# Optimization experiments

Hardware: AMD Instinct MI355X
Metric: run time of the kernel (lower is better)

The kernel has to match this reference:

```python
import jax, jax.numpy as jnp
import numpy as np

B, L, D, H, Dh = 4, 2048, 1024, 16, 64
DECAY_LR, A_LR, V_LR, G_LR = 64, 64, 32, 128
EPS_GN = 0.00064


def _lora(x, A, Bm, b, act):
    h = x @ A.T
    if act is not None:
        h = act(h)
    y = h @ Bm.T
    return y if b is None else y + b


def setup_inputs() -> dict:
    key = jax.random.key(0)
    ks = jax.random.split(key, 32)
    n = lambda k, shape, s=0.02: (jax.random.normal(k, shape, jnp.float32) * s)
    return {
        "x": n(ks[0], (B, L, D), 1.0),
        "v_first": n(ks[1], (B, L, H, Dh), 1.0),
        "x_r": n(ks[2], (1, 1, D)), "x_w": n(ks[3], (1, 1, D)),
        "x_k": n(ks[4], (1, 1, D)), "x_v": n(ks[5], (1, 1, D)),
        "x_a": n(ks[6], (1, 1, D)), "x_g": n(ks[7], (1, 1, D)),
        "k_k": n(ks[8], (H, Dh), 0.5), "k_a": n(ks[9], (H, Dh), 0.5),
        "r_k": n(ks[10], (H, Dh), 0.5),
        "Wr": n(ks[11], (D, D)), "Wk": n(ks[12], (D, D)),
        "Wv": n(ks[13], (D, D)), "Wo": n(ks[14], (D, D)),
        "gn_w": 1.0 + n(ks[15], (H, Dh)), "gn_b": n(ks[16], (H, Dh)),
        "w_A": n(ks[17], (DECAY_LR, D)), "w_B": n(ks[18], (D, DECAY_LR)), "w_b": n(ks[19], (D,)),
        "v_A": n(ks[20], (V_LR, D)), "v_B": n(ks[21], (D, V_LR)), "v_b": n(ks[22], (D,)),
        "a_A": n(ks[23], (A_LR, D)), "a_B": n(ks[24], (D, A_LR)), "a_b": n(ks[25], (D,)),
        "g_A": n(ks[26], (G_LR, D)), "g_B": n(ks[27], (D, G_LR)),
    }


def reference(x, v_first, x_r, x_w, x_k, x_v, x_a, x_g, k_k, k_a, r_k,
              Wr, Wk, Wv, Wo, gn_w, gn_b,
              w_A, w_B, w_b, v_A, v_B, v_b, a_A, a_B, a_b, g_A, g_B):
    Bx, Lx, Dx = x.shape
    # token shift (no cache -> zero-padded shift)
    x_prev = jnp.concatenate([jnp.zeros_like(x[:, :1]), x[:, :-1]], axis=1)
    xx = x_prev - x
    xr = x + xx * x_r
    xw = x + xx * x_w
    xk = x + xx * x_k
    xv = x + xx * x_v
    xa = x + xx * x_a
    xg = x + xx * x_g

    r = (xr @ Wr.T).reshape(Bx, Lx, H, Dh)
    k = (xk @ Wk.T).reshape(Bx, Lx, H, Dh)
    v = (xv @ Wv.T).reshape(Bx, Lx, H, Dh)
    iclr = jax.nn.sigmoid(_lora(xa, a_A, a_B, a_b, None)).reshape(Bx, Lx, H, Dh)
    gate = _lora(xg, g_A, g_B, None, jax.nn.sigmoid)  # (B,L,D)

    # layer_idx > 0: residual value mixing with v_first
    vv = jax.nn.sigmoid(_lora(xv, v_A, v_B, v_b, None)).reshape(Bx, Lx, H, Dh)
    v = v + (v_first - v) * vv

    w = jnp.exp(-0.606531 * jax.nn.sigmoid(
        _lora(xw, w_A, w_B, w_b, jnp.tanh)).reshape(Bx, Lx, H, Dh))

    kkn = k * k_k
    kk = kkn / jnp.maximum(jnp.linalg.norm(kkn, axis=-1, keepdims=True), 1e-7)
    k = k * (1.0 + (iclr - 1.0) * k_a)
    a = -kk
    b = kk * iclr

    # WKV7 generalized delta-rule scan over time
    def step(state, inp):
        rt, wt, kt, vt, at, bt = inp  # each (B,H,Dh)
        sa = jnp.einsum('bhij,bhj->bhi', state, at)
        state = (state * wt[:, :, None, :]
                 + vt[..., :, None] * kt[..., None, :]
                 + sa[..., :, None] * bt[..., None, :])
        y = jnp.einsum('bhij,bhj->bhi', state, rt)
        return state, y

    tr = lambda z: jnp.swapaxes(z, 0, 1)  # (B,L,H,Dh) -> (L,B,H,Dh)
    state0 = jnp.zeros((Bx, H, Dh, Dh), x.dtype)
    _, ys = jax.lax.scan(step, state0, (tr(r), tr(w), tr(k), tr(v), tr(a), tr(b)))
    out = jnp.swapaxes(ys, 0, 1)  # (B,L,H,Dh)

    # per-head layernorm (group norm), eps = 0.00064
    mean = out.mean(axis=-1, keepdims=True)
    var = out.var(axis=-1, keepdims=True)
    out = gn_w * (out - mean) / jnp.sqrt(var + EPS_GN) + gn_b

    out = out + jnp.sum(r * k * r_k, axis=-1, keepdims=True) * v
    out = out.reshape(Bx, Lx, Dx)
    return (out * gate) @ Wo.T
```

## Files before the change

### kernel.cpp

```cpp
#include <hip/hip_runtime.h>
#include <cmath>


#define DEV __device__ __forceinline__

typedef unsigned short u16;
typedef unsigned int u32;
typedef __bf16 bf16x8 __attribute__((ext_vector_type(8)));
typedef float f32x4 __attribute__((ext_vector_type(4)));

constexpr int Bx = 4, Lx = 2048, Dx = 1024, Hx = 16, Dh = 64;
constexpr int NTOK = Bx * Lx;
constexpr float EPS_GN = 0.00064f;
constexpr int STEP_U16 = 384;
constexpr int TB = 16;
constexpr int NB = Lx / TB;
constexpr int BATCH_U16 = TB * STEP_U16;

DEV float bf2f(u16 u) { union { u32 i; float f; } c; c.i = ((u32)u) << 16; return c.f; }
DEV u16 f2bf(float f) {
    union { float f; u32 i; } c; c.f = f;
    u32 r = c.i + 0x7FFFu + ((c.i >> 16) & 1u);
    return (u16)(r >> 16);
}
DEV void unpack2(u32 u, float& a, float& b) {
    union { u32 i; float f; } c0, c1;
    c0.i = u << 16; c1.i = u & 0xFFFF0000u;
    a = c0.f; b = c1.f;
}

template <int CTRL>
DEV float dpp_add(float v) {
    int p = __builtin_amdgcn_update_dpp(0, __float_as_int(v), CTRL, 0xF, 0xF, true);
    return v + __int_as_float(p);
}

DEV float xor32_add(float x) {
    float a = x, b = x;
    asm volatile("s_nop 1\n\tv_permlane32_swap_b32 %0, %1" : "+v"(a), "+v"(b));
    return a + b;
}

DEV float red32(float x) {
    x = dpp_add<0xB1>(x);
    x = dpp_add<0x4E>(x);
    x = dpp_add<0x141>(x);
    x = dpp_add<0x140>(x);
    return xor32_add(x);
}

__global__ __launch_bounds__(256) void convmix_kernel(
    const float* __restrict__ x,
    const float* __restrict__ mr, const float* __restrict__ mw, const float* __restrict__ mk,
    const float* __restrict__ mv, const float* __restrict__ ma, const float* __restrict__ mg,
    u16* __restrict__ XR, u16* __restrict__ XW, u16* __restrict__ XK,
    u16* __restrict__ XV, u16* __restrict__ XA, u16* __restrict__ XG,
    const float* s0, const float* s1, const float* s2, const float* s3,
    const float* s4, const float* s5, const float* s6, const float* s7,
    const float* s8, const float* s9, const float* s10, const float* s11,
    u16* d0, u16* d1, u16* d2, u16* d3, u16* d4, u16* d5, u16* d6, u16* d7,
    u16* d8, u16* d9, u16* d10, u16* d11)
{
    const int bid = blockIdx.x;
    const int tid = threadIdx.x;
    if (bid < 8192) {
        int gi = bid * 256 + tid;
        int n  = gi >> 8;
        int d4v = (gi & 255) << 2;
        int l  = n & (Lx - 1);
        size_t o = (size_t)n * Dx + d4v;
        float4 xc = *(const float4*)(x + o);
        float4 xp = make_float4(0.f, 0.f, 0.f, 0.f);
        if (l != 0) xp = *(const float4*)(x + o - Dx);
        float dx0 = xp.x - xc.x, dx1 = xp.y - xc.y, dx2 = xp.z - xc.z, dx3 = xp.w - xc.w;
        const float* mvs[6] = {mr, mw, mk, mv, ma, mg};
        u16* dsts[6] = {XR, XW, XK, XV, XA, XG};
#pragma unroll
        for (int j = 0; j < 6; ++j) {
            float4 m = *(const float4*)(mvs[j] + d4v);
            ushort4 r;
            r.x = f2bf(fmaf(dx0, m.x, xc.x));
            r.y = f2bf(fmaf(dx1, m.y, xc.y));
            r.z = f2bf(fmaf(dx2, m.z, xc.z));
            r.w = f2bf(fmaf(dx3, m.w, xc.w));
            *(ushort4*)(dsts[j] + o) = r;
        }
    } else {
        const float* srcs[12] = {s0,s1,s2,s3,s4,s5,s6,s7,s8,s9,s10,s11};
        u16* dsts[12] = {d0,d1,d2,d3,d4,d5,d6,d7,d8,d9,d10,d11};
        const int ns[12] = {65536,65536,32768,32768,65536,65536,131072,131072,
                            1048576,1048576,1048576,1048576};
        int cb = bid - 8192;
        int t = cb >> 10;
        int i = ((cb & 1023) * 256 + tid) * 4;
        if (i >= ns[t]) return;
        float4 v = *(const float4*)(srcs[t] + i);
        ushort4 o;
        o.x = f2bf(v.x); o.y = f2bf(v.y); o.z = f2bf(v.z); o.w = f2bf(v.w);
        *(ushort4*)(dsts[t] + i) = o;
    }
}

template <int BN, int ACT, bool BIAS, bool F32OUT>
DEV void gemm_body(u16* __restrict__ smem,
                   const u16* __restrict__ A, const u16* __restrict__ B16,
                   const float* __restrict__ bias, void* __restrict__ Cv,
                   int M, int N, int K, int bx, int by)
{
    constexpr int BM = 128, BK = 32;
    constexpr int WGM = (BN == 128) ? 2 : 4;
    constexpr int WGN = (BN == 128) ? 2 : 1;
    constexpr int WTM = BM / WGM, WTN = BN / WGN;
    constexpr int ITM = WTM / 16, ITN = WTN / 16;
    u16* Asm0 = smem;
    u16* Bsm0 = smem + 2 * BM * BK;
    const int tid = threadIdx.x;
    const int wid = tid >> 6, lane = tid & 63;
    const int q = lane >> 4, r16 = lane & 15;
    const size_t m0 = (size_t)bx * BM;
    const size_t n0 = (size_t)by * BN;
    const int wm = (wid % WGM) * WTM;
    const int wn = (wid / WGM) * WTN;
    f32x4 acc[ITM][ITN];
    const f32x4 zf = {0.f, 0.f, 0.f, 0.f};
#pragma unroll
    for (int i = 0; i < ITM; ++i)
#pragma unroll
        for (int j = 0; j < ITN; ++j) acc[i][j] = zf;

#pragma unroll
    for (int it = 0; it < 2; ++it) {
        int base = it * 2048 + wid * 512;
        int pp = base + lane * 8;
        int row = pp >> 5, col = pp & 31;
        __builtin_amdgcn_global_load_lds(
            (const __attribute__((address_space(1))) void*)(A + (m0 + row) * K + col),
            (__attribute__((address_space(3))) void*)(Asm0 + base), 16, 0, 0);
    }
#pragma unroll
    for (int it = 0; it < (BN * BK + 2047) / 2048; ++it) {
        int base = it * 2048 + wid * 512;
        if (BN * BK >= 2048 || base < BN * BK) {
            int pp = base + lane * 8;
            int row = pp >> 5, col = pp & 31;
            __builtin_amdgcn_global_load_lds(
                (const __attribute__((address_space(1))) void*)(B16 + (n0 + row) * K + col),
                (__attribute__((address_space(3))) void*)(Bsm0 + base), 16, 0, 0);
        }
    }

    int t = 0;
    for (int k0 = 0; k0 < K; k0 += BK, ++t) {
        const int cur = t & 1;
        __syncthreads();
        if (k0 + BK < K) {
            u16* An = Asm0 + (cur ^ 1) * (BM * BK);
            u16* Bn = Bsm0 + (cur ^ 1) * (BN * BK);
            const int kn = k0 + BK;
#pragma unroll
            for (int it = 0; it < 2; ++it) {
                int base = it * 2048 + wid * 512;
                int pp = base + lane * 8;
                int row = pp >> 5, col = pp & 31;
                __builtin_amdgcn_global_load_lds(
                    (const __attribute__((address_space(1))) void*)(A + (m0 + row) * K + kn + col),
                    (__attribute__((address_space(3))) void*)(An + base), 16, 0, 0);
            }
#pragma unroll
            for (int it = 0; it < (BN * BK + 2047) / 2048; ++it) {
                int base = it * 2048 + wid * 512;
                if (BN * BK >= 2048 || base < BN * BK) {
                    int pp = base + lane * 8;
                    int row = pp >> 5, col = pp & 31;
                    __builtin_amdgcn_global_load_lds(
                        (const __attribute__((address_space(1))) void*)(B16 + (n0 + row) * K + kn + col),
                        (__attribute__((address_space(3))) void*)(Bn + base), 16, 0, 0);
                }
            }
        }
        const u16* Ac = Asm0 + cur * (BM * BK);
        const u16* Bc = Bsm0 + cur * (BN * BK);
        bf16x8 af[ITM], bfr[ITN];
#pragma unroll
        for (int im = 0; im < ITM; ++im)
            af[im] = *(const bf16x8*)&Ac[(wm + im * 16 + r16) * BK + q * 8];
#pragma unroll
        for (int in = 0; in < ITN; ++in)
            bfr[in] = *(const bf16x8*)&Bc[(wn + in * 16 + r16) * BK + q * 8];
#pragma unroll
        for (int im = 0; im < ITM; ++im)
#pragma unroll
            for (int in = 0; in < ITN; ++in)
                acc[im][in] = __builtin_amdgcn_mfma_f32_16x16x32_bf16(af[im], bfr[in], acc[im][in], 0, 0, 0);
    }
#pragma unroll
    for (int im = 0; im < ITM; ++im) {
#pragma unroll
        for (int in = 0; in < ITN; ++in) {
#pragma unroll
            for (int e = 0; e < 4; ++e) {
                size_t row = m0 + wm + im * 16 + q * 4 + e;
                size_t col = n0 + wn + in * 16 + r16;
                float val = acc[im][in][e];
                if constexpr (BIAS) val += bias[col];
                if constexpr (ACT == 1) val = 1.f / (1.f + __expf(-val));
                else if constexpr (ACT == 2) val = tanhf(val);
                else if constexpr (ACT == 3) val = __expf(-0.606531f / (1.f + __expf(-val)));
                if constexpr (F32OUT) ((float*)Cv)[row * (size_t)N + col] = val;
                else ((u16*)Cv)[row * (size_t)N + col] = f2bf(val);
            }
        }
    }
}

DEV void gemm_body_rt(u16* __restrict__ smem,
                      const u16* __restrict__ A, const u16* __restrict__ B16,
                      const float* __restrict__ bias, u16* __restrict__ C,
                      int N, int K, int act, int bx, int by)
{
    constexpr int BM = 128, BK = 32;
    constexpr int ITM = 4, ITN = 4;
    u16* Asm0 = smem;
    u16* Bsm0 = smem + 2 * BM * BK;
    const int tid = threadIdx.x;
    const int wid = tid >> 6, lane = tid & 63;
    const int q = lane >> 4, r16 = lane & 15;
    const size_t m0 = (size_t)bx * BM;
    const size_t n0 = (size_t)by * 128;
    const int wm = (wid % 2) * 64;
    const int wn = (wid / 2) * 64;
    f32x4 acc[ITM][ITN];
    const f32x4 zf = {0.f, 0.f, 0.f, 0.f};
#pragma unroll
    for (int i = 0; i < ITM; ++i)
#pragma unroll
        for (int j = 0; j < ITN; ++j) acc[i][j] = zf;

#pragma unroll
    for (int it = 0; it < 2; ++it) {
        int base = it * 2048 + wid * 512;
        int pp = base + lane * 8;
        int row = pp >> 5, col = pp & 31;
        __builtin_amdgcn_global_load_lds(
            (const __attribute__((address_space(1))) void*)(A + (m0 + row) * K + col),
            (__attribute__((address_space(3))) void*)(Asm0 + base), 16, 0, 0);
        __builtin_amdgcn_global_load_lds(
            (const __attribute__((address_space(1))) void*)(B16 + (n0 + row) * K + col),
            (__attribute__((address_space(3))) void*)(Bsm0 + base), 16, 0, 0);
    }

    int t = 0;
    for (int k0 = 0; k0 < K; k0 += BK, ++t) {
        const int cur = t & 1;
        __syncthreads();
        if (k0 + BK < K) {
            u16* An = Asm0 + (cur ^ 1) * (BM * BK);
            u16* Bn = Bsm0 + (cur ^ 1) * (BM * BK);
            const int kn = k0 + BK;
#pragma unroll
            for (int it = 0; it < 2; ++it) {
                int base = it * 2048 + wid * 512;
                int pp = base + lane * 8;
                int row = pp >> 5, col = pp & 31;
                __builtin_amdgcn_global_load_lds(
                    (const __attribute__((address_space(1))) void*)(A + (m0 + row) * K + kn + col),
                    (__attribute__((address_space(3))) void*)(An + base), 16, 0, 0);
                __builtin_amdgcn_global_load_lds(
                    (const __attribute__((address_space(1))) void*)(B16 + (n0 + row) * K + kn + col),
                    (__attribute__((address_space(3))) void*)(Bn + base), 16, 0, 0);
            }
        }
        const u16* Ac = Asm0 + cur * (BM * BK);
        const u16* Bc = Bsm0 + cur * (BM * BK);
        bf16x8 af[ITM], bfr[ITN];
#pragma unroll
        for (int im = 0; im < ITM; ++im)
            af[im] = *(const bf16x8*)&Ac[(wm + im * 16 + r16) * BK + q * 8];
#pragma unroll
        for (int in = 0; in < ITN; ++in)
            bfr[in] = *(const bf16x8*)&Bc[(wn + in * 16 + r16) * BK + q * 8];
#pragma unroll
        for (int im = 0; im < ITM; ++im)
#pragma unroll
            for (int in = 0; in < ITN; ++in)
                acc[im][in] = __builtin_amdgcn_mfma_f32_16x16x32_bf16(af[im], bfr[in], acc[im][in], 0, 0, 0);
    }
#pragma unroll
    for (int im = 0; im < ITM; ++im) {
#pragma unroll
        for (int in = 0; in < ITN; ++in) {
#pragma unroll
            for (int e = 0; e < 4; ++e) {
                size_t row = m0 + wm + im * 16 + q * 4 + e;
                size_t col = n0 + wn + in * 16 + r16;
                float val = acc[im][in][e];
                if (bias) val += bias[col];
                if (act == 1) val = 1.f / (1.f + __expf(-val));
                else if (act == 3) val = __expf(-0.606531f / (1.f + __expf(-val)));
                C[row * (size_t)N + col] = f2bf(val);
            }
        }
    }
}

DEV void lora1_body(u16* __restrict__ smem, int cfg,
    const u16* __restrict__ XW, const u16* __restrict__ XA,
    const u16* __restrict__ XV, const u16* __restrict__ XG,
    const u16* __restrict__ wAB, const u16* __restrict__ aAB,
    const u16* __restrict__ vAB, const u16* __restrict__ gAB,
    u16* __restrict__ HW, u16* __restrict__ HA,
    u16* __restrict__ HV, u16* __restrict__ HG, int bx)
{
    constexpr int BM = 128, BK = 32, K = 1024;
    constexpr int ITM = 2, ITN = 4;
    const u16* A; const u16* Bm; u16* C; int ldC, Nv, act;
    if (cfg == 0)      { A = XW; Bm = wAB;            C = HW;      ldC = 64;  Nv = 64; act = 2; }
    else if (cfg == 1) { A = XA; Bm = aAB;            C = HA;      ldC = 64;  Nv = 64; act = 0; }
    else if (cfg == 2) { A = XV; Bm = vAB;            C = HV;      ldC = 32;  Nv = 32; act = 0; }
    else if (cfg == 3) { A = XG; Bm = gAB;            C = HG;      ldC = 128; Nv = 64; act = 1; }
    else               { A = XG; Bm = gAB + 64 * K;   C = HG + 64; ldC = 128; Nv = 64; act = 1; }

    u16* Asm0 = smem;
    u16* Bsm0 = smem + 2 * BM * BK;
    const int tid = threadIdx.x;
    const int wid = tid >> 6, lane = tid & 63;
    const int q = lane >> 4, r16 = lane & 15;
    const size_t m0 = (size_t)bx * BM;
    const int wm = wid * 32;
    f32x4 acc[ITM][ITN];
    const f32x4 zf = {0.f, 0.f, 0.f, 0.f};
#pragma unroll
    for (int i = 0; i < ITM; ++i)
#pragma unroll
        for (int j = 0; j < ITN; ++j) acc[i][j] = zf;

#pragma unroll
    for (int it = 0; it < 2; ++it) {
        int base = it * 2048 + wid * 512;
        int pp = base + lane * 8;
        int row = pp >> 5, col = pp & 31;
        __builtin_amdgcn_global_load_lds(
            (const __attribute__((address_space(1))) void*)(A + (m0 + row) * K + col),
            (__attribute__((address_space(3))) void*)(Asm0 + base), 16, 0, 0);
    }
    {
        int base = wid * 512;
        int pp = base + lane * 8;
        int row = pp >> 5, col = pp & 31;
        __builtin_amdgcn_global_load_lds(
            (const __attribute__((address_space(1))) void*)(Bm + row * K + col),
            (__attribute__((address_space(3))) void*)(Bsm0 + base), 16, 0, 0);
    }

    int t = 0;
    for (int k0 = 0; k0 < K; k0 += BK, ++t) {
        const int cur = t & 1;
        __syncthreads();
        if (k0 + BK < K) {
            u16* An = Asm0 + (cur ^ 1) * (BM * BK);
            u16* Bn = Bsm0 + (cur ^ 1) * 2048;
            const int kn = k0 + BK;
#pragma unroll
            for (int it = 0; it < 2; ++it) {
                int base = it * 2048 + wid * 512;
                int pp = base + lane * 8;
                int row = pp >> 5, col = pp & 31;
                __builtin_amdgcn_global_load_lds(
                    (const __attribute__((address_space(1))) void*)(A + (m0 + row) * K + kn + col),
                    (__attribute__((address_space(3))) void*)(An + base), 16, 0, 0);
            }
            {
                int base = wid * 512;
                int pp = base + lane * 8;
                int row = pp >> 5, col = pp & 31;
                __builtin_amdgcn_global_load_lds(
                    (const __attribute__((address_space(1))) void*)(Bm + row * K + kn + col),
                    (__attribute__((address_space(3))) void*)(Bn + base), 16, 0, 0);
            }
        }
        const u16* Ac = Asm0 + cur * (BM * BK);
        const u16* Bc = Bsm0 + cur * 2048;
        bf16x8 af[ITM], bfr[ITN];
#pragma unroll
        for (int im = 0; im < ITM; ++im)
            af[im] = *(const bf16x8*)&Ac[(wm + im * 16 + r16) * BK + q * 8];
#pragma unroll
        for (int in = 0; in < ITN; ++in)
            bfr[in] = *(const bf16x8*)&Bc[(in * 16 + r16) * BK + q * 8];
#pragma unroll
        for (int im = 0; im < ITM; ++im)
#pragma unroll
            for (int in = 0; in < ITN; ++in)
                acc[im][in] = __builtin_amdgcn_mfma_f32_16x16x32_bf16(af[im], bfr[in], acc[im][in], 0, 0, 0);
    }
#pragma unroll
    for (int im = 0; im < ITM; ++im) {
#pragma unroll
        for (int in = 0; in < ITN; ++in) {
#pragma unroll
            for (int e = 0; e < 4; ++e) {
                size_t row = m0 + wm + im * 16 + q * 4 + e;
                int col = in * 16 + r16;
                if (col < Nv) {
                    float val = acc[im][in][e];
                    if (act == 1) val = 1.f / (1.f + __expf(-val));
                    else if (act == 2) val = tanhf(val);
                    C[row * (size_t)ldC + col] = f2bf(val);
                }
            }
        }
    }
}

__global__ __launch_bounds__(256) void proj_kernel(
    const u16* __restrict__ XR, const u16* __restrict__ XK, const u16* __restrict__ XV,
    const u16* __restrict__ XW, const u16* __restrict__ XA, const u16* __restrict__ XG,
    const u16* __restrict__ Wr16, const u16* __restrict__ Wk16, const u16* __restrict__ Wv16,
    const u16* __restrict__ wAB, const u16* __restrict__ aAB,
    const u16* __restrict__ vAB, const u16* __restrict__ gAB,
    u16* __restrict__ Rbuf, u16* __restrict__ Kbuf, u16* __restrict__ Vbuf,
    u16* __restrict__ HW, u16* __restrict__ HA, u16* __restrict__ HV, u16* __restrict__ HG)
{
    __shared__ __align__(16) u16 pool[16384];
    const int z = blockIdx.z;
    if (z < 3) {
        const u16* A; const u16* Bm; u16* C;
        if (z == 0)      { A = XR; Bm = Wr16; C = Rbuf; }
        else if (z == 1) { A = XK; Bm = Wk16; C = Kbuf; }
        else             { A = XV; Bm = Wv16; C = Vbuf; }
        gemm_body<128, 0, false, false>(pool, A, Bm, nullptr, C, NTOK, 1024, 1024,
                                        blockIdx.x, blockIdx.y);
    } else {
        if (blockIdx.y >= 5) return;
        lora1_body(pool, blockIdx.y, XW, XA, XV, XG, wAB, aAB, vAB, gAB, HW, HA, HV, HG,
                   blockIdx.x);
    }
}

__global__ __launch_bounds__(256) void lora2_kernel(
    const u16* __restrict__ HW, const u16* __restrict__ HA,
    const u16* __restrict__ HV, const u16* __restrict__ HG,
    const u16* __restrict__ wBB, const u16* __restrict__ aBB,
    const u16* __restrict__ vBB, const u16* __restrict__ gBB,
    const float* __restrict__ wb, const float* __restrict__ ab, const float* __restrict__ vb,
    u16* __restrict__ Wdec16, u16* __restrict__ ICLR,
    u16* __restrict__ VVb, u16* __restrict__ GATE)
{
    __shared__ __align__(16) u16 pool[16384];
    const int z = blockIdx.z;
    const u16* A; const u16* Bm; const float* bias; u16* C; int K, act;
    if (z == 0)      { A = HW; Bm = wBB; bias = wb;      C = Wdec16; K = 64;  act = 3; }
    else if (z == 1) { A = HA; Bm = aBB; bias = ab;      C = ICLR;   K = 64;  act = 1; }
    else if (z == 2) { A = HV; Bm = vBB; bias = vb;      C = VVb;    K = 32;  act = 1; }
    else             { A = HG; Bm = gBB; bias = nullptr; C = GATE;   K = 128; act = 0; }
    gemm_body_rt(pool, A, Bm, bias, C, 1024, K, act, blockIdx.x, blockIdx.y);
}

__global__ __launch_bounds__(256) void gemm_out_kernel(
    const u16* __restrict__ A, const u16* __restrict__ B16, float* __restrict__ C)
{
    __shared__ __align__(16) u16 pool[16384];
    gemm_body<128, 0, false, true>(pool, A, B16, nullptr, C, NTOK, 1024, 1024,
                                   blockIdx.x, blockIdx.y);
}

__global__ __launch_bounds__(256) void prep_pack_kernel(
    const u16* __restrict__ Kb, const u16* __restrict__ Vb,
    const u16* __restrict__ Rb, const u16* __restrict__ Wd16,
    const u16* __restrict__ ICLR, const u16* __restrict__ VVb, const float* __restrict__ vfirst,
    const float* __restrict__ k_k, const float* __restrict__ k_a,
    u16* __restrict__ stream)
{
    int g = blockIdx.x * 4 + (threadIdx.x >> 6);
    int lane = threadIdx.x & 63;
    int h = g & (Hx - 1);
    int n = g >> 4;
    size_t idx = (size_t)g * 64 + lane;
    int hd = h * 64 + lane;
    int l = n & (Lx - 1), b = n >> 11;
    size_t so = ((size_t)((b * 16 + h) * Lx + l)) * STEP_U16;

    float k = bf2f(Kb[idx]);
    float iclr = bf2f(ICLR[idx]);
    float kkn = k * k_k[hd];
    float s = kkn * kkn;
#pragma unroll
    for (int off = 32; off > 0; off >>= 1) s += __shfl_xor(s, off, 64);
    float nrm = fmaxf(sqrtf(s), 1e-7f);
    float kk = kkn / nrm;
    u16 knew = f2bf(k * (1.f + (iclr - 1.f) * k_a[hd]));
    float v = bf2f(Vb[idx]), vv = bf2f(VVb[idx]), vf = vfirst[idx];
    u16 vnew = f2bf(fmaf(vf - v, vv, v));
    stream[so + lane]       = Rb[idx];
    stream[so + 64 + lane]  = knew;
    stream[so + 128 + lane] = f2bf(-kk);
    stream[so + 192 + lane] = f2bf(kk * iclr);
    stream[so + 256 + lane] = vnew;
    stream[so + 320 + lane] = Wd16[idx];
}

__global__ __launch_bounds__(256, 2) void scan_kernel(
    const u16* __restrict__ stream, float* __restrict__ Y)
{
    const int bid = blockIdx.x;
    const int xcd = bid & 7, slot = bid >> 3;
    const int bh = xcd + ((slot & 7) << 3);
    const int part = slot >> 3;
    const int tid = threadIdx.x;
    const int lane = tid & 63;
    const int w = tid >> 6;
    const int c = (lane & 15) | ((lane >> 1) & 16);
    const int rhalf = (lane >> 4) & 1;
    const int lr = w * 2 + rhalf;
    const int row = part * 8 + lr;
    const size_t sbase = (size_t)bh * Lx * STEP_U16;
    const size_t ybase = (size_t)(bh >> 4) * ((size_t)Lx * Dx) + (size_t)(bh & 15) * 64;

    __shared__ __align__(16) u16 sbuf[2 * BATCH_U16];
    __shared__ __align__(16) float yp[TB * 8 * 36];

    float S0 = 0.f, S1 = 0.f;

    {
        const u16* g = stream + sbase;
#pragma unroll
        for (int cc = 0; cc < 3; ++cc) {
            const u16* gp = g + (3 * w + cc) * 512 + lane * 8;
            u16* lp = sbuf + (3 * w + cc) * 512;
            __builtin_amdgcn_global_load_lds(
                (const __attribute__((address_space(1))) void*)gp,
                (__attribute__((address_space(3))) void*)lp, 16, 0, 0);
        }
    }

    for (int bt = 0; bt < NB; ++bt) {
        const int cur = bt & 1;
        __syncthreads();
        if (bt + 1 < NB) {
            const u16* g = stream + sbase + (size_t)(bt + 1) * BATCH_U16;
            u16* lbase = sbuf + (1 - cur) * BATCH_U16;
#pragma unroll
            for (int cc = 0; cc < 3; ++cc) {
                const u16* gp = g + (3 * w + cc) * 512 + lane * 8;
                u16* lp = lbase + (3 * w + cc) * 512;
                __builtin_amdgcn_global_load_lds(
                    (const __attribute__((address_space(1))) void*)gp,
                    (__attribute__((address_space(3))) void*)lp, 16, 0, 0);
            }
        }
        const u16* bp = sbuf + cur * BATCH_U16;
        const u16* cp = bp + c * 2;
        u32 r2 = *(const u32*)(cp);
        u32 k2 = *(const u32*)(cp + 64);
        u32 a2 = *(const u32*)(cp + 128);
        u32 b2 = *(const u32*)(cp + 192);
        u32 w2 = *(const u32*)(cp + 320);
        float v = bf2f(bp[256 + row]);
#pragma unroll
        for (int s = 0; s < TB; ++s) {
            u32 nr = 0, nk = 0, na = 0, nb = 0, nw = 0;
            float nv = 0.f;
            if (s + 1 < TB) {
                const u16* np = cp + (s + 1) * STEP_U16;
                nr = *(const u32*)(np);
                nk = *(const u32*)(np + 64);
                na = *(const u32*)(np + 128);
                nb = *(const u32*)(np + 192);
                nw = *(const u32*)(np + 320);
                nv = bf2f(bp[(s + 1) * STEP_U16 + 256 + row]);
            }
            float rr0, rr1, kk0, kk1, aa0, aa1, bb0, bb1, ww0, ww1;
            unpack2(r2, rr0, rr1);
            unpack2(k2, kk0, kk1);
            unpack2(a2, aa0, aa1);
            unpack2(b2, bb0, bb1);
            unpack2(w2, ww0, ww1);
            float sa = fmaf(S1, aa1, S0 * aa0);
            sa = red32(sa);
            float t0 = fmaf(v, kk0, sa * bb0);
            float t1 = fmaf(v, kk1, sa * bb1);
            S0 = fmaf(S0, ww0, t0);
            S1 = fmaf(S1, ww1, t1);
            float y = fmaf(S1, rr1, S0 * rr0);
            yp[(s * 8 + lr) * 36 + c] = y;
            r2 = nr; k2 = nk; a2 = na; b2 = nb; w2 = nw; v = nv;
        }
        __syncthreads();
        if (tid < TB * 8) {
            const float* rp = &yp[tid * 36];
            f32x4 a4 = *(const f32x4*)(rp);
#pragma unroll
            for (int i = 1; i < 8; ++i) {
                f32x4 t4 = *(const f32x4*)(rp + i * 4);
                a4 += t4;
            }
            float yy = (a4[0] + a4[1]) + (a4[2] + a4[3]);
            int s = tid >> 3, j = tid & 7;
            Y[ybase + (size_t)(bt * TB + s) * Dx + part * 8 + j] = yy;
        }
    }
}

__global__ __launch_bounds__(256) void gnorm_kernel(
    const float* __restrict__ Y, const u16* __restrict__ Rb,
    const u16* __restrict__ stream, const float* __restrict__ r_k,
    const float* __restrict__ gnw, const float* __restrict__ gnb,
    u16* __restrict__ GATE_OG)
{
    int g = blockIdx.x * 4 + (threadIdx.x >> 6);
    int lane = threadIdx.x & 63;
    int h = g & (Hx - 1);
    int n = g >> 4;
    size_t idx = (size_t)g * 64 + lane;
    int hd = h * 64 + lane;
    int l = n & (Lx - 1), b = n >> 11;
    size_t so = ((size_t)((b * 16 + h) * Lx + l)) * STEP_U16;
    float y = Y[idx];
    float r = bf2f(Rb[idx]);
    float k = bf2f(stream[so + 64 + lane]);
    float v = bf2f(stream[so + 256 + lane]);
    float rkr = r * k * r_k[hd];
    float s1 = y, s2 = y * y, s3 = rkr;
#pragma unroll
    for (int off = 32; off > 0; off >>= 1) {
        s1 += __shfl_xor(s1, off, 64);
        s2 += __shfl_xor(s2, off, 64);
        s3 += __shfl_xor(s3, off, 64);
    }
    float mean = s1 * (1.f / 64.f);
    float var  = s2 * (1.f / 64.f) - mean * mean;
    float inv = 1.f / sqrtf(var + EPS_GN);
    float o = gnw[hd] * ((y - mean) * inv) + gnb[hd];
    o += s3 * v;
    GATE_OG[idx] = f2bf(o * bf2f(GATE_OG[idx]));
}

extern "C" void kernel_launch(void* const* d_in, const int* in_sizes, int n_in,
                              void* d_out, int out_size, void* d_ws, size_t ws_size,
                              hipStream_t stream_)
{
    const float* x      = (const float*)d_in[0];
    const float* vfirst = (const float*)d_in[1];
    const float* x_r = (const float*)d_in[2];
    const float* x_w = (const float*)d_in[3];
    const float* x_k = (const float*)d_in[4];
    const float* x_v = (const float*)d_in[5];
    const float* x_a = (const float*)d_in[6];
    const float* x_g = (const float*)d_in[7];
    const float* k_k = (const float*)d_in[8];
    const float* k_a = (const float*)d_in[9];
    const float* r_k = (const float*)d_in[10];
    const float* Wr  = (const float*)d_in[11];
    const float* Wk  = (const float*)d_in[12];
    const float* Wv  = (const float*)d_in[13];
    const float* Wo  = (const float*)d_in[14];
    const float* gnw = (const float*)d_in[15];
    const float* gnb = (const float*)d_in[16];
    const float* wA  = (const float*)d_in[17];
    const float* wB  = (const float*)d_in[18];
    const float* wb  = (const float*)d_in[19];
    const float* vA  = (const float*)d_in[20];
    const float* vB  = (const float*)d_in[21];
    const float* vb  = (const float*)d_in[22];
    const float* aA  = (const float*)d_in[23];
    const float* aB  = (const float*)d_in[24];
    const float* ab  = (const float*)d_in[25];
    const float* gA  = (const float*)d_in[26];
    const float* gB  = (const float*)d_in[27];

    char* ws = (char*)d_ws;
    const size_t SLOT = (size_t)NTOK * Dx * 2;
    u16* XR = (u16*)(ws + 0 * SLOT);
    u16* XW = (u16*)(ws + 1 * SLOT);
    u16* XK = (u16*)(ws + 2 * SLOT);
    u16* XV = (u16*)(ws + 3 * SLOT);
    u16* XA = (u16*)(ws + 4 * SLOT);
    u16* XG = (u16*)(ws + 5 * SLOT);
    u16* STREAM = (u16*)(ws + 0 * SLOT);
    u16* Rbuf = (u16*)(ws + 6 * SLOT);
    u16* Kbuf = (u16*)(ws + 7 * SLOT);
    u16* Vbuf = (u16*)(ws + 8 * SLOT);
    u16* HW = (u16*)(ws + 9 * SLOT);
    u16* HA = HW + (size_t)NTOK * 64;
    u16* HV = HA + (size_t)NTOK * 64;
    u16* HG = HV + (size_t)NTOK * 32;
    u16* Wo16 = HG + (size_t)NTOK * 128;
    u16* SW = (u16*)(ws + 9 * SLOT + 8 * 1024 * 1024);
    u16* wAB = SW;
    u16* wBB = wAB + 65536;
    u16* vAB = wBB + 65536;
    u16* vBB = vAB + 32768;
    u16* aAB = vBB + 32768;
    u16* aBB = aAB + 65536;
    u16* gAB = aBB + 65536;
    u16* gBB = gAB + 131072;
    u16* Wr16 = (u16*)(ws + 9 * SLOT + 10 * 1024 * 1024);
    u16* Wk16 = Wr16 + 1048576;
    u16* Wv16 = Wk16 + 1048576;
    u16* Wdec16 = (u16*)(ws + 10 * SLOT);
    u16* ICLR   = (u16*)(ws + 11 * SLOT);
    u16* VVb    = (u16*)(ws + 12 * SLOT);
    float* Yb   = (float*)(ws + 10 * SLOT);
    u16* GATE   = (u16*)(ws + 13 * SLOT);

    dim3 blk(256);
    convmix_kernel<<<dim3(20480), blk, 0, stream_>>>(
        x, x_r, x_w, x_k, x_v, x_a, x_g, XR, XW, XK, XV, XA, XG,
        wA, wB, vA, vB, aA, aB, gA, gB, Wr, Wk, Wv, Wo,
        wAB, wBB, vAB, vBB, aAB, aBB, gAB, gBB, Wr16, Wk16, Wv16, Wo16);
    proj_kernel<<<dim3(64, 8, 4), blk, 0, stream_>>>(
        XR, XK, XV, XW, XA, XG, Wr16, Wk16, Wv16, wAB, aAB, vAB, gAB,
        Rbuf, Kbuf, Vbuf, HW, HA, HV, HG);
    lora2_kernel<<<dim3(64, 8, 4), blk, 0, stream_>>>(
        HW, HA, HV, HG, wBB, aBB, vBB, gBB, wb, ab, vb, Wdec16, ICLR, VVb, GATE);

    prep_pack_kernel<<<(NTOK * Hx) / 4, blk, 0, stream_>>>(Kbuf, Vbuf, Rbuf, Wdec16, ICLR, VVb,
                                                           vfirst, k_k, k_a, STREAM);
    scan_kernel<<<512, blk, 0, stream_>>>(STREAM, Yb);
    gnorm_kernel<<<(NTOK * Hx) / 4, blk, 0, stream_>>>(Yb, Rbuf, STREAM, r_k, gnw, gnb, GATE);
    gemm_out_kernel<<<dim3(64, 8), blk, 0, stream_>>>(GATE, Wo16, (float*)d_out);
}
```

Measured before the change: 691.3 us.

## Interleave r/k/a/b pairs in scan stream for 128-bit LDS loads, pack math

The per-step stream record is reorganised so that each column pair's r, k, a and b values sit contiguously as one 16-byte chunk, with w and v moved to new offsets. The scan kernel can then fetch four operands with a single uint4 LDS read instead of four separate 32-bit reads. The state update is rewritten with two-wide float vectors so the compiler can emit packed FMA instructions. The prep kernel now needs lane shuffles to interleave values before storing, and the gnorm kernel's k and v reads are updated to match the new layout.

```diff
diff --git a/kernel.cpp b/kernel.cpp
--- a/kernel.cpp
+++ b/kernel.cpp
@@ -8,6 +8,7 @@
 typedef unsigned int u32;
 typedef __bf16 bf16x8 __attribute__((ext_vector_type(8)));
 typedef float f32x4 __attribute__((ext_vector_type(4)));
+typedef float f32x2 __attribute__((ext_vector_type(2)));
 
 constexpr int Bx = 4, Lx = 2048, Dx = 1024, Hx = 16, Dh = 64;
 constexpr int NTOK = Bx * Lx;
@@ -23,10 +24,10 @@
     u32 r = c.i + 0x7FFFu + ((c.i >> 16) & 1u);
     return (u16)(r >> 16);
 }
-DEV void unpack2(u32 u, float& a, float& b) {
+DEV f32x2 up2(u32 u) {
     union { u32 i; float f; } c0, c1;
     c0.i = u << 16; c1.i = u & 0xFFFF0000u;
-    a = c0.f; b = c1.f;
+    f32x2 r; r.x = c0.f; r.y = c1.f; return r;
 }
 
 template <int CTRL>
@@ -491,12 +492,24 @@
     u16 knew = f2bf(k * (1.f + (iclr - 1.f) * k_a[hd]));
     float v = bf2f(Vb[idx]), vv = bf2f(VVb[idx]), vf = vfirst[idx];
     u16 vnew = f2bf(fmaf(vf - v, vv, v));
-    stream[so + lane]       = Rb[idx];
-    stream[so + 64 + lane]  = knew;
-    stream[so + 128 + lane] = f2bf(-kk);
-    stream[so + 192 + lane] = f2bf(kk * iclr);
-    stream[so + 256 + lane] = vnew;
-    stream[so + 320 + lane] = Wd16[idx];
+
+    int r_ = Rb[idx];        int r_p = __shfl_xor(r_, 1, 64);
+    int k_ = (int)knew;      int k_p = __shfl_xor(k_, 1, 64);
+    float a_ = -kk;          float a_p = __shfl_xor(a_, 1, 64);
+    float b_ = kk * iclr;    float b_p = __shfl_xor(b_, 1, 64);
+    int w_ = Wd16[idx];      int w_p = __shfl_xor(w_, 1, 64);
+    if ((lane & 1) == 0) {
+        int c = lane >> 1;
+        uint4 rkab;
+        rkab.x = (u32)(r_ & 0xFFFF) | ((u32)(r_p & 0xFFFF) << 16);
+        rkab.y = (u32)(k_ & 0xFFFF) | ((u32)(k_p & 0xFFFF) << 16);
+        rkab.z = (u32)f2bf(a_) | ((u32)f2bf(a_p) << 16);
+        rkab.w = (u32)f2bf(b_) | ((u32)f2bf(b_p) << 16);
+        *(uint4*)(stream + so + c * 8) = rkab;
+        *(u32*)(stream + so + 256 + c * 2) =
+            (u32)(w_ & 0xFFFF) | ((u32)(w_p & 0xFFFF) << 16);
+    }
+    stream[so + 320 + lane] = vnew;
 }
 
 __global__ __launch_bounds__(256, 2) void scan_kernel(
@@ -519,7 +532,7 @@
     __shared__ __align__(16) u16 sbuf[2 * BATCH_U16];
     __shared__ __align__(16) float yp[TB * 8 * 36];
 
-    float S0 = 0.f, S1 = 0.f;
+    f32x2 S = {0.f, 0.f};
 
     {
         const u16* g = stream + sbase;
@@ -549,41 +562,30 @@
             }
         }
         const u16* bp = sbuf + cur * BATCH_U16;
-        const u16* cp = bp + c * 2;
-        u32 r2 = *(const u32*)(cp);
-        u32 k2 = *(const u32*)(cp + 64);
-        u32 a2 = *(const u32*)(cp + 128);
-        u32 b2 = *(const u32*)(cp + 192);
-        u32 w2 = *(const u32*)(cp + 320);
-        float v = bf2f(bp[256 + row]);
+        const u16* cp = bp + c * 8;
+        const u16* wp = bp + 256 + c * 2;
+        uint4 rkab = *(const uint4*)cp;
+        u32 w2 = *(const u32*)wp;
+        float v = bf2f(bp[320 + row]);
 #pragma unroll
         for (int s = 0; s < TB; ++s) {
-            u32 nr = 0, nk = 0, na = 0, nb = 0, nw = 0;
-            float nv = 0.f;
+            uint4 nrkab = {0, 0, 0, 0}; u32 nw = 0; float nv = 0.f;
             if (s + 1 < TB) {
-                const u16* np = cp + (s + 1) * STEP_U16;
-                nr = *(const u32*)(np);
-                nk = *(const u32*)(np + 64);
-                na = *(const u32*)(np + 128);
-                nb = *(const u32*)(np + 192);
-                nw = *(const u32*)(np + 320);
-                nv = bf2f(bp[(s + 1) * STEP_U16 + 256 + row]);
-            }
-            float rr0, rr1, kk0, kk1, aa0, aa1, bb0, bb1, ww0, ww1;
-            unpack2(r2, rr0, rr1);
-            unpack2(k2, kk0, kk1);
-            unpack2(a2, aa0, aa1);
-            unpack2(b2, bb0, bb1);
-            unpack2(w2, ww0, ww1);
-            float sa = fmaf(S1, aa1, S0 * aa0);
+                nrkab = *(const uint4*)(cp + (s + 1) * STEP_U16);
+                nw = *(const u32*)(wp + (s + 1) * STEP_U16);
+                nv = bf2f(bp[(s + 1) * STEP_U16 + 320 + row]);
+            }
+            f32x2 rr = up2(rkab.x), kk = up2(rkab.y);
+            f32x2 aa = up2(rkab.z), bb = up2(rkab.w), ww = up2(w2);
+            f32x2 p = S * aa;
+            float sa = p.x + p.y;
             sa = red32(sa);
-            float t0 = fmaf(v, kk0, sa * bb0);
-            float t1 = fmaf(v, kk1, sa * bb1);
-            S0 = fmaf(S0, ww0, t0);
-            S1 = fmaf(S1, ww1, t1);
-            float y = fmaf(S1, rr1, S0 * rr0);
-            yp[(s * 8 + lr) * 36 + c] = y;
-            r2 = nr; k2 = nk; a2 = na; b2 = nb; w2 = nw; v = nv;
+            f32x2 sav = {sa, sa}, vv2 = {v, v};
+            S = __builtin_elementwise_fma(S, ww,
+                    __builtin_elementwise_fma(vv2, kk, sav * bb));
+            f32x2 q = S * rr;
+            yp[(s * 8 + lr) * 36 + c] = q.x + q.y;
+            rkab = nrkab; w2 = nw; v = nv;
         }
         __syncthreads();
         if (tid < TB * 8) {
@@ -617,8 +619,8 @@
     size_t so = ((size_t)((b * 16 + h) * Lx + l)) * STEP_U16;
     float y = Y[idx];
     float r = bf2f(Rb[idx]);
-    float k = bf2f(stream[so + 64 + lane]);
-    float v = bf2f(stream[so + 256 + lane]);
+    float k = bf2f(stream[so + (lane >> 1) * 8 + 2 + (lane & 1)]);
+    float v = bf2f(stream[so + 320 + lane]);
     float rkr = r * k * r_k[hd];
     float s1 = y, s2 = y * y, s3 = rkr;
 #pragma unroll
```

Result: no change. 691.2 us (-0.0%).
